# Optimization experiments

Measured on AMD Instinct MI355X. Metric: run time of the kernel, lower is better.

## Reference

```python
import jax, jax.numpy as jnp
import numpy as np

N_NODES = 100000
NEG_SLOPE = 0.2


def gat_conv(x, edge_index, W, a_src, a_dst, bias):
    """PyG GATConv, heads=1, concat, add_self_loops=True."""
    N = x.shape[0]
    loop = jnp.arange(N, dtype=edge_index.dtype)
    src = jnp.concatenate([edge_index[0], loop])  # message sources j
    dst = jnp.concatenate([edge_index[1], loop])  # message targets i
    h = x @ W                                      # [N, out]
    asrc = h @ a_src                               # [N]
    adst = h @ a_dst                               # [N]
    e = jax.nn.leaky_relu(asrc[src] + adst[dst], NEG_SLOPE)   # [E+N]
    m = jax.ops.segment_max(e, dst, num_segments=N)           # per-dst max
    w = jnp.exp(e - jax.lax.stop_gradient(m)[dst])
    denom = jax.ops.segment_sum(w, dst, num_segments=N)
    alpha = w / denom[dst]                                     # softmax per dst
    out = jax.ops.segment_sum(alpha[:, None] * h[src], dst, num_segments=N)
    return out + bias


def setup_inputs() -> dict:
    key = jax.random.key(0)
    ks = jax.random.split(key, 16)
    N, E, D = N_NODES, 3200000, 128
    x = jax.random.normal(ks[0], (N, D), dtype=jnp.float32)
    edge_index = jax.random.randint(ks[1], (2, E), 0, N, dtype=jnp.int64)
    def glorot(k, shape):
        fan = sum(shape)
        return jax.random.uniform(k, shape, jnp.float32, -1.0, 1.0) * np.sqrt(6.0 / fan)
    return {
        "x": x,
        "edge_index": edge_index,
        "W1": glorot(ks[2], (D, 16)),
        "a1_src": glorot(ks[3], (16,)),
        "a1_dst": glorot(ks[4], (16,)),
        "b1": jnp.zeros((16,), jnp.float32),
        "W2": glorot(ks[5], (16, 10)),
        "a2_src": glorot(ks[6], (10,)),
        "a2_dst": glorot(ks[7], (10,)),
        "b2": jnp.zeros((10,), jnp.float32),
        "Wl1": glorot(ks[8], (10, 10)),
        "bl1": jnp.zeros((10,), jnp.float32),
        "Wl2": glorot(ks[9], (10, 1)),
        "bl2": jnp.zeros((1,), jnp.float32),
    }


def reference(x, edge_index, W1, a1_src, a1_dst, b1, W2, a2_src, a2_dst, b2,
              Wl1, bl1, Wl2, bl2):
    h = gat_conv(x, edge_index, W1, a1_src, a1_dst, b1)
    h = jax.nn.relu(h)
    h = gat_conv(h, edge_index, W2, a2_src, a2_dst, b2)
    h = h @ Wl1 + bl1
    h = jax.nn.relu(h)
    return h @ Wl2 + bl2  # [N, 1]
```

## Files before the change

kernel.cpp:

```cpp
#include <hip/hip_runtime.h>
#include <hip/hip_fp16.h>


#define NEG 0.2f
#define FSH 7
#define BNODES 128
#define NSBMAX 1024
#define CAPB 4608
#define TILE 8192
#define PES 9

__device__ __forceinline__ float lrelu(float x) { return x > 0.0f ? x : NEG * x; }

__device__ __forceinline__ unsigned fenc(float f) {
    unsigned u = __float_as_uint(f);
    return (u & 0x80000000u) ? ~u : (u | 0x80000000u);
}
__device__ __forceinline__ float fdec(unsigned e) {
    return (e & 0x80000000u) ? __uint_as_float(e & 0x7FFFFFFFu) : __uint_as_float(~e);
}

__device__ __forceinline__ float4 ldh4(const __half* h, size_t off) {
    uint2 u = *(const uint2*)(h + off);
    __half2 a = *(__half2*)&u.x, b = *(__half2*)&u.y;
    float2 fa = __half22float2(a), fb = __half22float2(b);
    return make_float4(fa.x, fa.y, fb.x, fb.y);
}

__global__ __launch_bounds__(256) void k_init(unsigned* g, int* bcur, int NSB) {
    int i = blockIdx.x * 256 + threadIdx.x;
    if (i < NSB) bcur[i * 16] = i * CAPB;
    if (i < 2) g[i] = 0u;
}

__global__ __launch_bounds__(256) void k_gemm1(
    const float* __restrict__ x, const float* __restrict__ W1,
    const float* __restrict__ a1s, const float* __restrict__ a1d,
    __half* __restrict__ h1, float* __restrict__ s1, float* __restrict__ d1,
    unsigned* __restrict__ gmax, int N)
{
    __shared__ float sW[128 * 16];
    __shared__ float sx[64 * 132];
    __shared__ float wm[4];
    int tid = threadIdx.x;
    for (int i = tid; i < 2048; i += 256) sW[i] = W1[i];
    int node0 = blockIdx.x * 64;
    for (int i = tid; i < 64 * 32; i += 256) {
        int row = i >> 5, c4 = i & 31;
        int n = node0 + row;
        float4 v = make_float4(0.f, 0.f, 0.f, 0.f);
        if (n < N) v = ((const float4*)x)[(size_t)n * 32 + c4];
        *(float4*)&sx[row * 132 + c4 * 4] = v;
    }
    __syncthreads();

    int node = node0 + (tid >> 2);
    int grp  = tid & 3;
    const float* xr = &sx[(tid >> 2) * 132];
    float4 acc = make_float4(0.f, 0.f, 0.f, 0.f);
#pragma unroll 8
    for (int j = 0; j < 128; ++j) {
        float xv = xr[j];
        float4 w = *(const float4*)&sW[j * 16 + grp * 4];
        acc.x += xv * w.x; acc.y += xv * w.y; acc.z += xv * w.z; acc.w += xv * w.w;
    }
    float4 as = ((const float4*)a1s)[grp];
    float4 ad = ((const float4*)a1d)[grp];
    float sv = acc.x * as.x + acc.y * as.y + acc.z * as.z + acc.w * as.w;
    float dv = acc.x * ad.x + acc.y * ad.y + acc.z * ad.z + acc.w * ad.w;
    sv += __shfl_xor(sv, 1); sv += __shfl_xor(sv, 2);
    dv += __shfl_xor(dv, 1); dv += __shfl_xor(dv, 2);
    if (node < N) {
        __half2 p0 = __floats2half2_rn(acc.x, acc.y);
        __half2 p1 = __floats2half2_rn(acc.z, acc.w);
        uint2 u; u.x = *(unsigned*)&p0; u.y = *(unsigned*)&p1;
        *(uint2*)&h1[(size_t)node * 16 + grp * 4] = u;
        if (grp == 0) { s1[node] = sv; d1[node] = dv; }
    }
    float m = (node < N) ? sv : -3.4e38f;
#pragma unroll
    for (int off = 32; off >= 1; off >>= 1) m = fmaxf(m, __shfl_xor(m, off));
    if ((tid & 63) == 0) wm[tid >> 6] = m;
    __syncthreads();
    if (tid == 0) {
        float b = fmaxf(fmaxf(wm[0], wm[1]), fmaxf(wm[2], wm[3]));
        atomicMax(gmax, fenc(b));
    }
}

__global__ __launch_bounds__(512) void k_csplit(
    const int* __restrict__ esrc, const int* __restrict__ edst,
    int* __restrict__ bcur, unsigned* __restrict__ pairs, int E, int NSB)
{
    __shared__ unsigned lsrt[TILE];
    __shared__ int lhist[NSBMAX];
    __shared__ int lofs[NSBMAX];
    __shared__ int gbase[NSBMAX];
    __shared__ int wsum[8];
    int tid = threadIdx.x;
    int base = blockIdx.x * TILE;
    int tcnt = min(TILE, E - base);
    for (int i = tid; i < NSB; i += 512) lhist[i] = 0;
    __syncthreads();
    for (int i = tid; i < tcnt; i += 512)
        atomicAdd(&lhist[edst[base + i] >> FSH], 1);
    __syncthreads();
    int i0 = 2 * tid, i1 = i0 + 1;
    int a = (i0 < NSB) ? lhist[i0] : 0;
    int b = (i1 < NSB) ? lhist[i1] : 0;
    int s = a + b, pfx = s;
#pragma unroll
    for (int off = 1; off < 64; off <<= 1) {
        int t = __shfl_up(pfx, off, 64);
        if ((tid & 63) >= off) pfx += t;
    }
    if ((tid & 63) == 63) wsum[tid >> 6] = pfx;
    __syncthreads();
    int carry = 0;
    for (int w = 0; w < (tid >> 6); ++w) carry += wsum[w];
    int excl = pfx + carry - s;
    if (i0 < NSB) {
        lofs[i0] = excl;
        gbase[i0] = a ? atomicAdd(&bcur[i0 * 16], a) : 0;
    }
    if (i1 < NSB) {
        lofs[i1] = excl + a;
        gbase[i1] = b ? atomicAdd(&bcur[i1 * 16], b) : 0;
    }
    __syncthreads();
    if (i0 < NSB) lhist[i0] = lofs[i0];
    if (i1 < NSB) lhist[i1] = lofs[i1];
    __syncthreads();
    for (int i = tid; i < tcnt; i += 512) {
        int e = base + i;
        int d = edst[e], srcv = esrc[e];
        int pos = atomicAdd(&lhist[d >> FSH], 1);
        lsrt[pos] = ((unsigned)(d & (BNODES - 1)) << 17) | (unsigned)srcv;
    }
    __syncthreads();
    for (int i = tid; i < tcnt; i += 512) {
        int lo = 0, hi = NSB - 1;
        while (lo < hi) { int mid = (lo + hi + 1) >> 1; if (lofs[mid] <= i) lo = mid; else hi = mid - 1; }
        int gp = gbase[lo] + (i - lofs[lo]);
        if (gp < (lo + 1) * CAPB) pairs[gp] = lsrt[i];
    }
}

__global__ __launch_bounds__(512) void k_agg1(
    const int* __restrict__ bcur, const unsigned* __restrict__ pairs,
    const int* __restrict__ esrc, const int* __restrict__ edst,
    const float* __restrict__ s1, const float* __restrict__ d1, const __half* __restrict__ h1,
    const float* __restrict__ b1, const float* __restrict__ W2,
    const float* __restrict__ a2s, const float* __restrict__ a2d,
    __half* __restrict__ h2, float* __restrict__ s2, float* __restrict__ d2,
    const unsigned* __restrict__ gmax1p, unsigned* __restrict__ gmax2, int N, int E)
{
    __shared__ unsigned srt[CAPB];
    __shared__ float accs[BNODES * 17];
    __shared__ int lcnt[BNODES];
    __shared__ int lofs[BNODES + 1];
    __shared__ float dds[BNODES], mbs[BNODES];
    __shared__ float sW[160], sb[16], sas[16], sad[16];
    __shared__ int wsum[8];
    __shared__ float wm[8];

    int tid = threadIdx.x;
    int fb = blockIdx.x;
    if (tid < 160) sW[tid] = W2[tid];
    if (tid < 16) {
        sb[tid]  = b1[tid];
        sas[tid] = (tid < 10) ? a2s[tid] : 0.f;
        sad[tid] = (tid < 10) ? a2d[tid] : 0.f;
    }
    int node0 = fb << FSH;
    float g0 = fdec(*gmax1p);
    if (tid < BNODES) {
        int n = node0 + tid;
        float dd = (n < N) ? d1[n] : 0.f;
        dds[tid] = dd; mbs[tid] = lrelu(g0 + dd);
        lcnt[tid] = 0;
    }
    __syncthreads();

    int rbase = fb * CAPB;
    int cnt = bcur[fb * 16] - rbase;
    int gg = tid >> 2, q = tid & 3;

    if (cnt <= CAPB) {
        unsigned pe[PES];
#pragma unroll
        for (int u = 0; u < PES; ++u) {
            int i = tid + u * 512;
            bool ok = (i < cnt);
            pe[u] = ok ? pairs[rbase + i] : 0u;
            if (ok) atomicAdd(&lcnt[(pe[u] >> 17) & (BNODES - 1)], 1);
        }
        __syncthreads();
        int c = (tid < BNODES) ? lcnt[tid] : 0;
        int pfx = c;
#pragma unroll
        for (int off = 1; off < 64; off <<= 1) {
            int t = __shfl_up(pfx, off, 64);
            if ((tid & 63) >= off) pfx += t;
        }
        if ((tid & 63) == 63) wsum[tid >> 6] = pfx;
        __syncthreads();
        int carry = 0;
        for (int w = 0; w < (tid >> 6); ++w) carry += wsum[w];
        pfx += carry;
        if (tid < BNODES) { lofs[tid + 1] = pfx; lcnt[tid] = pfx - c; }
        if (tid == 0) lofs[0] = 0;
        __syncthreads();
#pragma unroll
        for (int u = 0; u < PES; ++u) {
            int i = tid + u * 512;
            if (i < cnt) {
                unsigned p = pe[u];
                int pos = atomicAdd(&lcnt[(p >> 17) & (BNODES - 1)], 1);
                srt[pos] = p & 0x1FFFF;
            }
        }
        __syncthreads();

        int n = node0 + gg;
        float4 accv; float den;
        if (n < N) {
            float w = __expf(lrelu(s1[n] + dds[gg]) - mbs[gg]);
            float4 hv = ldh4(h1, (size_t)n * 16 + 4 * q);
            accv = make_float4(w * hv.x, w * hv.y, w * hv.z, w * hv.w);
            den = w;
        } else { accv = make_float4(0.f, 0.f, 0.f, 0.f); den = 0.f; }
        {
            float dd = dds[gg], mb = mbs[gg];
            int j = lofs[gg], j1 = lofs[gg + 1];
            for (; j + 4 <= j1; j += 4) {
                int e0 = srt[j], e1 = srt[j + 1], e2 = srt[j + 2], e3 = srt[j + 3];
                float4 H0 = ldh4(h1, (size_t)e0 * 16 + 4 * q);
                float4 H1 = ldh4(h1, (size_t)e1 * 16 + 4 * q);
                float4 H2 = ldh4(h1, (size_t)e2 * 16 + 4 * q);
                float4 H3 = ldh4(h1, (size_t)e3 * 16 + 4 * q);
                int eq = srt[j + q];
                float wq = __expf(lrelu(s1[eq] + dd) - mb);
                float w0 = __shfl(wq, 0, 4), w1 = __shfl(wq, 1, 4);
                float w2 = __shfl(wq, 2, 4), w3 = __shfl(wq, 3, 4);
                accv.x += w0 * H0.x + w1 * H1.x + w2 * H2.x + w3 * H3.x;
                accv.y += w0 * H0.y + w1 * H1.y + w2 * H2.y + w3 * H3.y;
                accv.z += w0 * H0.z + w1 * H1.z + w2 * H2.z + w3 * H3.z;
                accv.w += w0 * H0.w + w1 * H1.w + w2 * H2.w + w3 * H3.w;
                den += (w0 + w1) + (w2 + w3);
            }
            for (; j < j1; ++j) {
                int e0 = srt[j];
                float w0 = __expf(lrelu(s1[e0] + dd) - mb);
                float4 H0 = ldh4(h1, (size_t)e0 * 16 + 4 * q);
                accv.x += w0 * H0.x; accv.y += w0 * H0.y;
                accv.z += w0 * H0.z; accv.w += w0 * H0.w;
                den += w0;
            }
        }
        accs[gg * 17 + 4 * q + 0] = accv.x;
        accs[gg * 17 + 4 * q + 1] = accv.y;
        accs[gg * 17 + 4 * q + 2] = accv.z;
        accs[gg * 17 + 4 * q + 3] = accv.w;
        if (q == 0) accs[gg * 17 + 16] = den;
        __syncthreads();
    } else {
        for (int i = tid; i < BNODES * 17; i += 512) accs[i] = 0.f;
        __syncthreads();
        if (tid < BNODES) {
            int n = node0 + tid;
            if (n < N) {
                float w = __expf(lrelu(s1[n] + dds[tid]) - mbs[tid]);
#pragma unroll
                for (int t = 0; t < 16; ++t)
                    accs[tid * 17 + t] = w * __half2float(h1[(size_t)n * 16 + t]);
                accs[tid * 17 + 16] = w;
            }
        }
        __syncthreads();
        for (int i = tid; i < E; i += 512) {
            int d = edst[i];
            if ((d >> FSH) != fb) continue;
            int nl = d & (BNODES - 1), src = esrc[i];
            float w = __expf(lrelu(s1[src] + dds[nl]) - mbs[nl]);
#pragma unroll
            for (int t = 0; t < 16; ++t)
                atomicAdd(&accs[nl * 17 + t], w * __half2float(h1[(size_t)src * 16 + t]));
            atomicAdd(&accs[nl * 17 + 16], w);
        }
        __syncthreads();
    }

    int g = tid >> 4, k = tid & 15;
    float sval = -3.4e38f;
#pragma unroll
    for (int qq = 0; qq < 4; ++qq) {
        int nl = g * 4 + qq, nn = node0 + nl;
        if (nn >= N) continue;
        float inv = 1.f / accs[nl * 17 + 16];
        float o = fmaxf(accs[nl * 17 + k] * inv + sb[k], 0.f);
        float hh = 0.f;
#pragma unroll
        for (int kk = 0; kk < 16; ++kk) {
            float ov = __shfl(o, kk, 16);
            if (k < 10) hh += ov * sW[kk * 10 + k];
        }
        if (k >= 10) hh = 0.f;
        float ts = hh * sas[k];
        float td = hh * sad[k];
#pragma unroll
        for (int off = 1; off < 16; off <<= 1) {
            ts += __shfl_xor(ts, off, 16);
            td += __shfl_xor(td, off, 16);
        }
        h2[(size_t)nn * 16 + k] = __float2half_rn(hh);
        if (k == 0) { s2[nn] = ts; d2[nn] = td; }
        sval = fmaxf(sval, ts);
    }
    float m = sval;
#pragma unroll
    for (int off = 32; off >= 1; off >>= 1) m = fmaxf(m, __shfl_xor(m, off));
    if ((tid & 63) == 0) wm[tid >> 6] = m;
    __syncthreads();
    if (tid == 0) {
        float bmx = wm[0];
#pragma unroll
        for (int i = 1; i < 8; ++i) bmx = fmaxf(bmx, wm[i]);
        atomicMax(gmax2, fenc(bmx));
    }
}

__global__ __launch_bounds__(512) void k_agg2(
    const int* __restrict__ bcur, const unsigned* __restrict__ pairs,
    const int* __restrict__ esrc, const int* __restrict__ edst,
    const float* __restrict__ s2, const float* __restrict__ d2, const __half* __restrict__ h2,
    const float* __restrict__ b2, const float* __restrict__ Wl1, const float* __restrict__ bl1,
    const float* __restrict__ Wl2, const float* __restrict__ bl2,
    const unsigned* __restrict__ gmax2p, float* __restrict__ out, int N, int E)
{
    __shared__ unsigned srt[CAPB];
    __shared__ float accs[BNODES * 17];
    __shared__ int lcnt[BNODES];
    __shared__ int lofs[BNODES + 1];
    __shared__ float dds[BNODES], mbs[BNODES];
    __shared__ float sW1[100], sb1[16], sW2[16], sb2g[16];
    __shared__ float sbl2;
    __shared__ int wsum[8];

    int tid = threadIdx.x;
    int fb = blockIdx.x;
    if (tid < 100) sW1[tid] = Wl1[tid];
    if (tid < 16) {
        sb1[tid]  = (tid < 10) ? bl1[tid] : 0.f;
        sW2[tid]  = (tid < 10) ? Wl2[tid] : 0.f;
        sb2g[tid] = (tid < 10) ? b2[tid]  : 0.f;
    }
    if (tid == 0) sbl2 = bl2[0];
    int node0 = fb << FSH;
    float g0 = fdec(*gmax2p);
    if (tid < BNODES) {
        int n = node0 + tid;
        float dd = (n < N) ? d2[n] : 0.f;
        dds[tid] = dd; mbs[tid] = lrelu(g0 + dd);
        lcnt[tid] = 0;
    }
    __syncthreads();

    int rbase = fb * CAPB;
    int cnt = bcur[fb * 16] - rbase;
    int gg = tid >> 2, q = tid & 3;

    if (cnt <= CAPB) {
        unsigned pe[PES];
#pragma unroll
        for (int u = 0; u < PES; ++u) {
            int i = tid + u * 512;
            bool ok = (i < cnt);
            pe[u] = ok ? pairs[rbase + i] : 0u;
            if (ok) atomicAdd(&lcnt[(pe[u] >> 17) & (BNODES - 1)], 1);
        }
        __syncthreads();
        int c = (tid < BNODES) ? lcnt[tid] : 0;
        int pfx = c;
#pragma unroll
        for (int off = 1; off < 64; off <<= 1) {
            int t = __shfl_up(pfx, off, 64);
            if ((tid & 63) >= off) pfx += t;
        }
        if ((tid & 63) == 63) wsum[tid >> 6] = pfx;
        __syncthreads();
        int carry = 0;
        for (int w = 0; w < (tid >> 6); ++w) carry += wsum[w];
        pfx += carry;
        if (tid < BNODES) { lofs[tid + 1] = pfx; lcnt[tid] = pfx - c; }
        if (tid == 0) lofs[0] = 0;
        __syncthreads();
#pragma unroll
        for (int u = 0; u < PES; ++u) {
            int i = tid + u * 512;
            if (i < cnt) {
                unsigned p = pe[u];
                int pos = atomicAdd(&lcnt[(p >> 17) & (BNODES - 1)], 1);
                srt[pos] = p & 0x1FFFF;
            }
        }
        __syncthreads();

        int n = node0 + gg;
        float4 accv; float den;
        if (n < N) {
            float w = __expf(lrelu(s2[n] + dds[gg]) - mbs[gg]);
            float4 hv = ldh4(h2, (size_t)n * 16 + 4 * q);
            accv = make_float4(w * hv.x, w * hv.y, w * hv.z, w * hv.w);
            den = w;
        } else { accv = make_float4(0.f, 0.f, 0.f, 0.f); den = 0.f; }
        {
            float dd = dds[gg], mb = mbs[gg];
            int j = lofs[gg], j1 = lofs[gg + 1];
            for (; j + 4 <= j1; j += 4) {
                int e0 = srt[j], e1 = srt[j + 1], e2 = srt[j + 2], e3 = srt[j + 3];
                float4 H0 = ldh4(h2, (size_t)e0 * 16 + 4 * q);
                float4 H1 = ldh4(h2, (size_t)e1 * 16 + 4 * q);
                float4 H2 = ldh4(h2, (size_t)e2 * 16 + 4 * q);
                float4 H3 = ldh4(h2, (size_t)e3 * 16 + 4 * q);
                int eq = srt[j + q];
                float wq = __expf(lrelu(s2[eq] + dd) - mb);
                float w0 = __shfl(wq, 0, 4), w1 = __shfl(wq, 1, 4);
                float w2 = __shfl(wq, 2, 4), w3 = __shfl(wq, 3, 4);
                accv.x += w0 * H0.x + w1 * H1.x + w2 * H2.x + w3 * H3.x;
                accv.y += w0 * H0.y + w1 * H1.y + w2 * H2.y + w3 * H3.y;
                accv.z += w0 * H0.z + w1 * H1.z + w2 * H2.z + w3 * H3.z;
                accv.w += w0 * H0.w + w1 * H1.w + w2 * H2.w + w3 * H3.w;
                den += (w0 + w1) + (w2 + w3);
            }
            for (; j < j1; ++j) {
                int e0 = srt[j];
                float w0 = __expf(lrelu(s2[e0] + dd) - mb);
                float4 H0 = ldh4(h2, (size_t)e0 * 16 + 4 * q);
                accv.x += w0 * H0.x; accv.y += w0 * H0.y;
                accv.z += w0 * H0.z; accv.w += w0 * H0.w;
                den += w0;
            }
        }
        accs[gg * 17 + 4 * q + 0] = accv.x;
        accs[gg * 17 + 4 * q + 1] = accv.y;
        accs[gg * 17 + 4 * q + 2] = accv.z;
        accs[gg * 17 + 4 * q + 3] = accv.w;
        if (q == 0) accs[gg * 17 + 16] = den;
        __syncthreads();
    } else {
        for (int i = tid; i < BNODES * 17; i += 512) accs[i] = 0.f;
        __syncthreads();
        if (tid < BNODES) {
            int n = node0 + tid;
            if (n < N) {
                float w = __expf(lrelu(s2[n] + dds[tid]) - mbs[tid]);
#pragma unroll
                for (int t = 0; t < 16; ++t)
                    accs[tid * 17 + t] = w * __half2float(h2[(size_t)n * 16 + t]);
                accs[tid * 17 + 16] = w;
            }
        }
        __syncthreads();
        for (int i = tid; i < E; i += 512) {
            int d = edst[i];
            if ((d >> FSH) != fb) continue;
            int nl = d & (BNODES - 1), src = esrc[i];
            float w = __expf(lrelu(s2[src] + dds[nl]) - mbs[nl]);
#pragma unroll
            for (int t = 0; t < 16; ++t)
                atomicAdd(&accs[nl * 17 + t], w * __half2float(h2[(size_t)src * 16 + t]));
            atomicAdd(&accs[nl * 17 + 16], w);
        }
        __syncthreads();
    }

    int g = tid >> 4, k = tid & 15;
    bool fk = k < 10;
#pragma unroll
    for (int qq = 0; qq < 4; ++qq) {
        int nl = g * 4 + qq, nn = node0 + nl;
        if (nn >= N) continue;
        float inv = 1.f / accs[nl * 17 + 16];
        float o = fk ? accs[nl * 17 + k] * inv + sb2g[k] : 0.f;
        float v = sb1[k];
#pragma unroll
        for (int kk = 0; kk < 10; ++kk) {
            float ov = __shfl(o, kk, 16);
            if (fk) v += ov * sW1[kk * 10 + k];
        }
        float t = fmaxf(v, 0.f);
        float cc = t * sW2[k];
#pragma unroll
        for (int off = 1; off < 16; off <<= 1) cc += __shfl_xor(cc, off, 16);
        if (k == 0) out[nn] = cc + sbl2;
    }
}

extern "C" void kernel_launch(void* const* d_in, const int* in_sizes, int n_in,
                              void* d_out, int out_size, void* d_ws, size_t ws_size,
                              hipStream_t stream)
{
    const float* x   = (const float*)d_in[0];
    const int*   ei  = (const int*)  d_in[1];
    const float* W1  = (const float*)d_in[2];
    const float* a1s = (const float*)d_in[3];
    const float* a1d = (const float*)d_in[4];
    const float* b1  = (const float*)d_in[5];
    const float* W2  = (const float*)d_in[6];
    const float* a2s = (const float*)d_in[7];
    const float* a2d = (const float*)d_in[8];
    const float* b2  = (const float*)d_in[9];
    const float* Wl1 = (const float*)d_in[10];
    const float* bl1 = (const float*)d_in[11];
    const float* Wl2 = (const float*)d_in[12];
    const float* bl2 = (const float*)d_in[13];

    int N = in_sizes[0] / 128;
    int E = in_sizes[1] / 2;
    const int* ei_src = ei;
    const int* ei_dst = ei + E;
    int NSB = (N + BNODES - 1) >> FSH;

    size_t Np = ((size_t)N + 3) & ~(size_t)3;
    size_t need_bytes = (16 + Np * 20) * 4 + (size_t)NSB * 16 * 4 + (size_t)NSB * CAPB * 4;
    if (ws_size < need_bytes) return;

    float*    ws    = (float*)d_ws;
    unsigned* gmax1 = (unsigned*)d_ws;
    unsigned* gmax2 = gmax1 + 1;
    __half* h1 = (__half*)(ws + 16);
    float* s1 = ws + 16 + Np * 8;
    float* d1 = s1 + Np;
    __half* h2 = (__half*)(d1 + Np);
    float* s2 = (float*)(h2) + Np * 8;
    float* d2 = s2 + Np;
    int* bcur = (int*)(d2 + Np);
    unsigned* pairs = (unsigned*)(bcur + (size_t)NSB * 16);

    hipLaunchKernelGGL(k_init, dim3((NSB + 255) / 256), dim3(256), 0, stream, gmax1, bcur, NSB);
    hipLaunchKernelGGL(k_gemm1, dim3((N + 63) / 64), dim3(256), 0, stream,
                       x, W1, a1s, a1d, h1, s1, d1, gmax1, N);
    hipLaunchKernelGGL(k_csplit, dim3((E + TILE - 1) / TILE), dim3(512), 0, stream,
                       ei_src, ei_dst, bcur, pairs, E, NSB);
    hipLaunchKernelGGL(k_agg1, dim3(NSB), dim3(512), 0, stream,
                       bcur, pairs, ei_src, ei_dst, s1, d1, h1, b1, W2, a2s, a2d,
                       h2, s2, d2, gmax1, gmax2, N, E);
    hipLaunchKernelGGL(k_agg2, dim3(NSB), dim3(512), 0, stream,
                       bcur, pairs, ei_src, ei_dst, s2, d2, h2, b2, Wl1, bl1, Wl2, bl2,
                       gmax2, (float*)d_out, N, E);
}
```

Measured before the change: 277.9 us.

## Merge gemm1 and edge bucketing into one interleaved front kernel

Combines the dense feature GEMM and the edge counting-sort split into a single launch whose blocks are interleaved between the two roles, so the compute-bound GEMM and the memory-bound scatter can overlap on the GPU. The init kernel is replaced with a memset, and bucket cursors now start at zero and are stored relative to each bucket. The split tile is halved to 4096 edges with 256 threads to fit the shared-memory union. This saves launches and idle tails, but the two roles become more imbalanced per block and the scatter writes are less coalesced.

```diff
diff --git a/kernel.cpp b/kernel.cpp
--- a/kernel.cpp
+++ b/kernel.cpp
@@ -7,7 +7,7 @@
 #define BNODES 128
 #define NSBMAX 1024
 #define CAPB 4608
-#define TILE 8192
+#define TILE 4096
 #define PES 9
 
 __device__ __forceinline__ float lrelu(float x) { return x > 0.0f ? x : NEG * x; }
@@ -27,24 +27,84 @@
     return make_float4(fa.x, fa.y, fb.x, fb.y);
 }
 
-__global__ __launch_bounds__(256) void k_init(unsigned* g, int* bcur, int NSB) {
-    int i = blockIdx.x * 256 + threadIdx.x;
-    if (i < NSB) bcur[i * 16] = i * CAPB;
-    if (i < 2) g[i] = 0u;
-}
-
-__global__ __launch_bounds__(256) void k_gemm1(
+__global__ __launch_bounds__(256) void k_front(
     const float* __restrict__ x, const float* __restrict__ W1,
     const float* __restrict__ a1s, const float* __restrict__ a1d,
     __half* __restrict__ h1, float* __restrict__ s1, float* __restrict__ d1,
-    unsigned* __restrict__ gmax, int N)
+    unsigned* __restrict__ gmax,
+    const int* __restrict__ esrc, const int* __restrict__ edst,
+    int* __restrict__ bcur, unsigned* __restrict__ pairs,
+    int N, int E, int NG, int NC, int NSB)
 {
-    __shared__ float sW[128 * 16];
-    __shared__ float sx[64 * 132];
-    __shared__ float wm[4];
+    __shared__ float smem[10500];
     int tid = threadIdx.x;
+    int bid = blockIdx.x;
+    long long T = (long long)NG + NC;
+    int before = (int)(((long long)bid * NC) / T);
+    int isc = (int)((((long long)bid + 1) * NC) / T) > before;
+
+    if (isc) {
+        unsigned* lsrt = (unsigned*)smem;
+        int* lhist = (int*)smem + TILE;
+        int* lofs  = lhist + NSBMAX;
+        int* gbase = lofs + NSBMAX;
+        int* wsum  = gbase + NSBMAX;
+        int cid = before;
+        int base = cid * TILE;
+        int tcnt = min(TILE, E - base);
+        for (int i = tid; i < NSB; i += 256) lhist[i] = 0;
+        __syncthreads();
+        for (int i = tid; i < tcnt; i += 256)
+            atomicAdd(&lhist[edst[base + i] >> FSH], 1);
+        __syncthreads();
+        int i0 = 4 * tid;
+        int a0 = (i0 + 0 < NSB) ? lhist[i0 + 0] : 0;
+        int a1 = (i0 + 1 < NSB) ? lhist[i0 + 1] : 0;
+        int a2 = (i0 + 2 < NSB) ? lhist[i0 + 2] : 0;
+        int a3 = (i0 + 3 < NSB) ? lhist[i0 + 3] : 0;
+        int s = a0 + a1 + a2 + a3, pfx = s;
+#pragma unroll
+        for (int off = 1; off < 64; off <<= 1) {
+            int t = __shfl_up(pfx, off, 64);
+            if ((tid & 63) >= off) pfx += t;
+        }
+        if ((tid & 63) == 63) wsum[tid >> 6] = pfx;
+        __syncthreads();
+        int carry = 0;
+        for (int w = 0; w < (tid >> 6); ++w) carry += wsum[w];
+        int excl = pfx + carry - s;
+        if (i0 + 0 < NSB) { lofs[i0 + 0] = excl;                 gbase[i0 + 0] = a0 ? atomicAdd(&bcur[(i0 + 0) * 16], a0) : 0; }
+        if (i0 + 1 < NSB) { lofs[i0 + 1] = excl + a0;            gbase[i0 + 1] = a1 ? atomicAdd(&bcur[(i0 + 1) * 16], a1) : 0; }
+        if (i0 + 2 < NSB) { lofs[i0 + 2] = excl + a0 + a1;       gbase[i0 + 2] = a2 ? atomicAdd(&bcur[(i0 + 2) * 16], a2) : 0; }
+        if (i0 + 3 < NSB) { lofs[i0 + 3] = excl + a0 + a1 + a2;  gbase[i0 + 3] = a3 ? atomicAdd(&bcur[(i0 + 3) * 16], a3) : 0; }
+        __syncthreads();
+        if (i0 + 0 < NSB) lhist[i0 + 0] = lofs[i0 + 0];
+        if (i0 + 1 < NSB) lhist[i0 + 1] = lofs[i0 + 1];
+        if (i0 + 2 < NSB) lhist[i0 + 2] = lofs[i0 + 2];
+        if (i0 + 3 < NSB) lhist[i0 + 3] = lofs[i0 + 3];
+        __syncthreads();
+        for (int i = tid; i < tcnt; i += 256) {
+            int e = base + i;
+            int d = edst[e], srcv = esrc[e];
+            int pos = atomicAdd(&lhist[d >> FSH], 1);
+            lsrt[pos] = ((unsigned)(d & (BNODES - 1)) << 17) | (unsigned)srcv;
+        }
+        __syncthreads();
+        for (int i = tid; i < tcnt; i += 256) {
+            int lo = 0, hi = NSB - 1;
+            while (lo < hi) { int mid = (lo + hi + 1) >> 1; if (lofs[mid] <= i) lo = mid; else hi = mid - 1; }
+            int rel = gbase[lo] + (i - lofs[lo]);
+            if (rel < CAPB) pairs[(size_t)lo * CAPB + rel] = lsrt[i];
+        }
+        return;
+    }
+
+    float* sW = smem;
+    float* sx = smem + 2048;
+    float* wm = smem + 2048 + 64 * 132;
+    int gid = bid - before;
     for (int i = tid; i < 2048; i += 256) sW[i] = W1[i];
-    int node0 = blockIdx.x * 64;
+    int node0 = gid * 64;
     for (int i = tid; i < 64 * 32; i += 256) {
         int row = i >> 5, c4 = i & 31;
         int n = node0 + row;
@@ -85,64 +145,6 @@
     if (tid == 0) {
         float b = fmaxf(fmaxf(wm[0], wm[1]), fmaxf(wm[2], wm[3]));
         atomicMax(gmax, fenc(b));
-    }
-}
-
-__global__ __launch_bounds__(512) void k_csplit(
-    const int* __restrict__ esrc, const int* __restrict__ edst,
-    int* __restrict__ bcur, unsigned* __restrict__ pairs, int E, int NSB)
-{
-    __shared__ unsigned lsrt[TILE];
-    __shared__ int lhist[NSBMAX];
-    __shared__ int lofs[NSBMAX];
-    __shared__ int gbase[NSBMAX];
-    __shared__ int wsum[8];
-    int tid = threadIdx.x;
-    int base = blockIdx.x * TILE;
-    int tcnt = min(TILE, E - base);
-    for (int i = tid; i < NSB; i += 512) lhist[i] = 0;
-    __syncthreads();
-    for (int i = tid; i < tcnt; i += 512)
-        atomicAdd(&lhist[edst[base + i] >> FSH], 1);
-    __syncthreads();
-    int i0 = 2 * tid, i1 = i0 + 1;
-    int a = (i0 < NSB) ? lhist[i0] : 0;
-    int b = (i1 < NSB) ? lhist[i1] : 0;
-    int s = a + b, pfx = s;
-#pragma unroll
-    for (int off = 1; off < 64; off <<= 1) {
-        int t = __shfl_up(pfx, off, 64);
-        if ((tid & 63) >= off) pfx += t;
-    }
-    if ((tid & 63) == 63) wsum[tid >> 6] = pfx;
-    __syncthreads();
-    int carry = 0;
-    for (int w = 0; w < (tid >> 6); ++w) carry += wsum[w];
-    int excl = pfx + carry - s;
-    if (i0 < NSB) {
-        lofs[i0] = excl;
-        gbase[i0] = a ? atomicAdd(&bcur[i0 * 16], a) : 0;
-    }
-    if (i1 < NSB) {
-        lofs[i1] = excl + a;
-        gbase[i1] = b ? atomicAdd(&bcur[i1 * 16], b) : 0;
-    }
-    __syncthreads();
-    if (i0 < NSB) lhist[i0] = lofs[i0];
-    if (i1 < NSB) lhist[i1] = lofs[i1];
-    __syncthreads();
-    for (int i = tid; i < tcnt; i += 512) {
-        int e = base + i;
-        int d = edst[e], srcv = esrc[e];
-        int pos = atomicAdd(&lhist[d >> FSH], 1);
-        lsrt[pos] = ((unsigned)(d & (BNODES - 1)) << 17) | (unsigned)srcv;
-    }
-    __syncthreads();
-    for (int i = tid; i < tcnt; i += 512) {
-        int lo = 0, hi = NSB - 1;
-        while (lo < hi) { int mid = (lo + hi + 1) >> 1; if (lofs[mid] <= i) lo = mid; else hi = mid - 1; }
-        int gp = gbase[lo] + (i - lofs[lo]);
-        if (gp < (lo + 1) * CAPB) pairs[gp] = lsrt[i];
     }
 }
 
@@ -183,7 +185,7 @@
     __syncthreads();
 
     int rbase = fb * CAPB;
-    int cnt = bcur[fb * 16] - rbase;
+    int cnt = bcur[fb * 16];
     int gg = tid >> 2, q = tid & 3;
 
     if (cnt <= CAPB) {
@@ -367,7 +369,7 @@
     __syncthreads();
 
     int rbase = fb * CAPB;
-    int cnt = bcur[fb * 16] - rbase;
+    int cnt = bcur[fb * 16];
     int gg = tid >> 2, q = tid & 3;
 
     if (cnt <= CAPB) {
@@ -523,26 +525,28 @@
     int NSB = (N + BNODES - 1) >> FSH;
 
     size_t Np = ((size_t)N + 3) & ~(size_t)3;
-    size_t need_bytes = (16 + Np * 20) * 4 + (size_t)NSB * 16 * 4 + (size_t)NSB * CAPB * 4;
+    size_t need_bytes = (16 + (size_t)NSB * 16) * 4 + Np * 20 * 4 + (size_t)NSB * CAPB * 4;
     if (ws_size < need_bytes) return;
 
-    float*    ws    = (float*)d_ws;
     unsigned* gmax1 = (unsigned*)d_ws;
     unsigned* gmax2 = gmax1 + 1;
-    __half* h1 = (__half*)(ws + 16);
-    float* s1 = ws + 16 + Np * 8;
+    int* bcur = (int*)d_ws + 16;
+    float* rest = (float*)d_ws + 16 + (size_t)NSB * 16;
+    __half* h1 = (__half*)rest;
+    float* s1 = rest + Np * 8;
     float* d1 = s1 + Np;
     __half* h2 = (__half*)(d1 + Np);
     float* s2 = (float*)(h2) + Np * 8;
     float* d2 = s2 + Np;
-    int* bcur = (int*)(d2 + Np);
-    unsigned* pairs = (unsigned*)(bcur + (size_t)NSB * 16);
-
-    hipLaunchKernelGGL(k_init, dim3((NSB + 255) / 256), dim3(256), 0, stream, gmax1, bcur, NSB);
-    hipLaunchKernelGGL(k_gemm1, dim3((N + 63) / 64), dim3(256), 0, stream,
-                       x, W1, a1s, a1d, h1, s1, d1, gmax1, N);
-    hipLaunchKernelGGL(k_csplit, dim3((E + TILE - 1) / TILE), dim3(512), 0, stream,
-                       ei_src, ei_dst, bcur, pairs, E, NSB);
+    unsigned* pairs = (unsigned*)(d2 + Np);
+
+    int NG = (N + 63) / 64;
+    int NC = (E + TILE - 1) / TILE;
+
+    hipMemsetAsync(d_ws, 0, (16 + (size_t)NSB * 16) * sizeof(int), stream);
+    hipLaunchKernelGGL(k_front, dim3(NG + NC), dim3(256), 0, stream,
+                       x, W1, a1s, a1d, h1, s1, d1, gmax1,
+                       ei_src, ei_dst, bcur, pairs, N, E, NG, NC, NSB);
     hipLaunchKernelGGL(k_agg1, dim3(NSB), dim3(512), 0, stream,
                        bcur, pairs, ei_src, ei_dst, s1, d1, h1, b1, W2, a2s, a2d,
                        h2, s2, d2, gmax1, gmax2, N, E);
```

Result: no change. 279.1 us (+0.4%).
